# Kernel tuning notes

Measured on AMD Instinct MI355X. Metric: run time of the kernel, lower is better.

Reference implementation:

```python
import jax, jax.numpy as jnp
import numpy as np

N_NODES = 100000
N_EDGES = 1600000
IN_C, HID_C, OUT_C = 128, 128, 64


def gcn_conv(x, src, dst, n_nodes, W, b):
    # PyG GCNConv (normalize=True, add_self_loops=True):
    # out = D^{-1/2} (A+I) D^{-1/2} (x @ W^T) + b
    h = x @ W.T                                   # [N, out]
    deg = jax.ops.segment_sum(jnp.ones(src.shape, x.dtype), dst,
                              num_segments=n_nodes)  # includes self-loops
    dinv = jnp.where(deg > 0, jax.lax.rsqrt(deg), 0.0)
    norm = dinv[src] * dinv[dst]                  # [E+N]
    msg = h[src] * norm[:, None]                  # gather + scale
    out = jax.ops.segment_sum(msg, dst, num_segments=n_nodes)
    return out + b


def setup_inputs() -> dict:
    key = jax.random.key(0)
    ks = jax.random.split(key, 8)
    x = jax.random.normal(ks[0], (N_NODES, IN_C), dtype=jnp.float32)
    edge_index = jax.random.randint(ks[1], (2, N_EDGES), 0, N_NODES, dtype=jnp.int64)

    def lin(k, fan_out, fan_in):
        s = 1.0 / np.sqrt(fan_in)
        kw, kb = jax.random.split(k)
        W = jax.random.uniform(kw, (fan_out, fan_in), jnp.float32, -s, s)
        b = jax.random.uniform(kb, (fan_out,), jnp.float32, -s, s)
        return W, b

    W1, b1 = lin(ks[2], HID_C, IN_C)
    W2, b2 = lin(ks[3], HID_C, HID_C)
    W3, b3 = lin(ks[4], OUT_C, HID_C)
    return {"x": x, "edge_index": edge_index,
            "W1": W1, "b1": b1, "W2": W2, "b2": b2, "W3": W3, "b3": b3}


def reference(x, edge_index, W1, b1, W2, b2, W3, b3):
    n = x.shape[0]
    loop = jnp.arange(n, dtype=edge_index.dtype)
    src = jnp.concatenate([edge_index[0], loop])  # add self-loops once; identical per layer
    dst = jnp.concatenate([edge_index[1], loop])
    h = gcn_conv(x, src, dst, n, W1, b1)
    h = jax.nn.relu(h)
    h = gcn_conv(h, src, dst, n, W2, b2)
    h = jax.nn.relu(h)
    h = gcn_conv(h, src, dst, n, W3, b3)
    return h
```

## Files before the change

kernel.cpp:

```cpp
#include <hip/hip_runtime.h>


#define NPB 256
#define CAP 4672
#define BIN_WGS 512

typedef short bfrag __attribute__((ext_vector_type(8)));
typedef float f32x4 __attribute__((ext_vector_type(4)));
typedef unsigned short u16x8 __attribute__((ext_vector_type(8)));

__global__ __launch_bounds__(256) void init_cur(int* __restrict__ cur, int B) {
  int i = blockIdx.x * 256 + threadIdx.x;
  if (i < B) cur[i] = i * CAP;
}

__global__ __launch_bounds__(256) void bin_edges(const int* __restrict__ src,
                                                 const int* __restrict__ dst,
                                                 int* __restrict__ cur,
                                                 int* __restrict__ binned,
                                                 int E, int B) {
  __shared__ int lc[512];
  __shared__ int lbase[512];
  const int t = threadIdx.x;
  const int chunk = (E + BIN_WGS - 1) / BIN_WGS;
  const int e0 = blockIdx.x * chunk;
  const int e1 = min(E, e0 + chunk);

  for (int i = t; i < B; i += 256) lc[i] = 0;
  __syncthreads();
  for (int e = e0 + t; e < e1; e += 256) {
    int d = dst[e];
    atomicAdd(&lc[d >> 8], 1);
  }
  __syncthreads();
  for (int i = t; i < B; i += 256) {
    int c = lc[i];
    lbase[i] = c ? atomicAdd(&cur[i], c) : 0;
    lc[i] = 0;
  }
  __syncthreads();
  for (int e = e0 + t; e < e1; e += 256) {
    int d = dst[e];
    int s = __builtin_nontemporal_load(&src[e]);
    int bk = d >> 8;
    int p = lbase[bk] + atomicAdd(&lc[bk], 1);
    if (p < (bk + 1) * CAP)
      binned[p] = ((d & 255) << 24) | s;
  }
}

__global__ __launch_bounds__(256) void build_buckets(const int* __restrict__ binned,
                                                     const int* __restrict__ cur,
                                                     int* __restrict__ cols,
                                                     int2* __restrict__ off2,
                                                     float* __restrict__ dinv,
                                                     int N) {
  __shared__ int eb[CAP];
  __shared__ int ob[CAP];
  __shared__ int lc[256];
  __shared__ int sc[256];
  const int b = blockIdx.x;
  const int t = threadIdx.x;
  const int base = b * CAP;
  const int cntb = min(cur[b] - base, CAP);

  for (int i = t; i < cntb; i += 256) eb[i] = binned[base + i];
  lc[t] = 0;
  __syncthreads();
  for (int i = t; i < cntb; i += 256)
    atomicAdd(&lc[(unsigned)eb[i] >> 24], 1);
  __syncthreads();
  int myc = lc[t];
  sc[t] = myc;
  __syncthreads();
  for (int d = 1; d < 256; d <<= 1) {
    int a = (t >= d) ? sc[t - d] : 0;
    __syncthreads();
    sc[t] += a;
    __syncthreads();
  }
  int excl = sc[t] - myc;
  int node = b * NPB + t;
  if (node < N) {
    off2[node] = make_int2(base + excl, base + excl + myc);
    dinv[node] = rsqrtf((float)(myc + 1));
  }
  lc[t] = excl;
  __syncthreads();
  for (int i = t; i < cntb; i += 256) {
    int e = eb[i];
    int p = atomicAdd(&lc[(unsigned)e >> 24], 1);
    ob[p] = e & 0xFFFFFF;
  }
  __syncthreads();
  for (int i = t; i < cntb; i += 256) cols[base + i] = ob[i];
}

__device__ inline unsigned short bf16rne(float x) {
  unsigned u = __float_as_uint(x);
  return (unsigned short)((u + 0x7FFFu + ((u >> 16) & 1u)) >> 16);
}
__device__ inline float bf16lo(unsigned q) { return __uint_as_float(q << 16); }
__device__ inline float bf16hi(unsigned q) { return __uint_as_float(q & 0xFFFF0000u); }

__global__ __launch_bounds__(256) void split_w3(const float* __restrict__ W1,
                                                const float* __restrict__ W2,
                                                const float* __restrict__ W3,
                                                unsigned short* __restrict__ w1h,
                                                unsigned short* __restrict__ w1l,
                                                unsigned short* __restrict__ w2h,
                                                unsigned short* __restrict__ w2l,
                                                unsigned short* __restrict__ w3h,
                                                unsigned short* __restrict__ w3l) {
  int i = blockIdx.x * 256 + threadIdx.x;
  const float* W;
  unsigned short *hi, *lo;
  int j;
  if (i < 16384) {
    W = W1; hi = w1h; lo = w1l; j = i;
  } else if (i < 32768) {
    W = W2; hi = w2h; lo = w2l; j = i - 16384;
  } else if (i < 40960) {
    W = W3; hi = w3h; lo = w3l; j = i - 32768;
  } else {
    return;
  }
  float v = W[j];
  unsigned short h = bf16rne(v);
  hi[j] = h;
  lo[j] = bf16rne(v - __uint_as_float((unsigned)h << 16));
}

__global__ __launch_bounds__(256) void split_x(const float* __restrict__ X,
                                               unsigned short* __restrict__ xh,
                                               unsigned short* __restrict__ xl,
                                               int total8) {
  int i = blockIdx.x * 256 + threadIdx.x;
  if (i >= total8) return;
  const float4* px = (const float4*)(X + (size_t)i * 8);
  float4 v0 = px[0], v1 = px[1];
  float vv[8] = {v0.x, v0.y, v0.z, v0.w, v1.x, v1.y, v1.z, v1.w};
  u16x8 hv, lv;
#pragma unroll
  for (int j = 0; j < 8; ++j) {
    unsigned short h = bf16rne(vv[j]);
    hv[j] = h;
    lv[j] = bf16rne(vv[j] - __uint_as_float((unsigned)h << 16));
  }
  __builtin_nontemporal_store(hv, (u16x8*)(xh + (size_t)i * 8));
  __builtin_nontemporal_store(lv, (u16x8*)(xl + (size_t)i * 8));
}

#define LDP 136
template <int OUTC>
__global__ __launch_bounds__(256) void gemm_planes(const unsigned short* __restrict__ Xh,
                                                   const unsigned short* __restrict__ Xl,
                                                   const unsigned short* __restrict__ Whg,
                                                   const unsigned short* __restrict__ Wlg,
                                                   const float* __restrict__ dinv,
                                                   unsigned short* __restrict__ Y,
                                                   int M) {
  constexpr int CHUNKS = OUTC / 64;
  __shared__ unsigned short Whi[64 * LDP], Wlo[64 * LDP];
  const int tid = threadIdx.x;
  const int bx = blockIdx.x;
  const int m_base = (bx / CHUNKS) * 64;
  const int cc = (bx % CHUNKS) * 64;

  for (int idx = tid; idx < 64 * 16; idx += 256) {
    int r = idx >> 4, g = idx & 15;
    *(u16x8*)(Whi + r * LDP + g * 8) =
        *(const u16x8*)(Whg + (size_t)(cc + r) * 128 + g * 8);
    *(u16x8*)(Wlo + r * LDP + g * 8) =
        *(const u16x8*)(Wlg + (size_t)(cc + r) * 128 + g * 8);
  }
  __syncthreads();

  const int lane = tid & 63;
  const int wv = tid >> 6;
  const int col_l = lane & 15;
  const int quad = lane >> 4;
  const size_t arow = (size_t)min(m_base + wv * 16 + col_l, M - 1) * 128;
  const int bBase = col_l * LDP + quad * 8;

  bfrag aH[4], aL[4];
#pragma unroll
  for (int ks = 0; ks < 4; ++ks) {
    aH[ks] = *(const bfrag*)(Xh + arow + ks * 32 + quad * 8);
    aL[ks] = *(const bfrag*)(Xl + arow + ks * 32 + quad * 8);
  }

  f32x4 acc[4] = {{0.f, 0.f, 0.f, 0.f},
                  {0.f, 0.f, 0.f, 0.f},
                  {0.f, 0.f, 0.f, 0.f},
                  {0.f, 0.f, 0.f, 0.f}};
#pragma unroll
  for (int ks = 0; ks < 4; ++ks) {
#pragma unroll
    for (int t = 0; t < 4; ++t) {
      int bo = bBase + t * 16 * LDP + ks * 32;
      bfrag bHi = *(const bfrag*)(Whi + bo);
      bfrag bLo = *(const bfrag*)(Wlo + bo);
      acc[t] = __builtin_amdgcn_mfma_f32_16x16x32_bf16(aH[ks], bHi, acc[t], 0, 0, 0);
      acc[t] = __builtin_amdgcn_mfma_f32_16x16x32_bf16(aL[ks], bHi, acc[t], 0, 0, 0);
      acc[t] = __builtin_amdgcn_mfma_f32_16x16x32_bf16(aH[ks], bLo, acc[t], 0, 0, 0);
    }
  }

#pragma unroll
  for (int r = 0; r < 4; ++r) {
    int row = m_base + wv * 16 + quad * 4 + r;
    if (row < M) {
      float s = dinv[row];
#pragma unroll
      for (int t = 0; t < 4; ++t) {
        unsigned short h = bf16rne(acc[t][r] * s);
        Y[(size_t)row * OUTC + cc + t * 16 + col_l] = h;
      }
    }
  }
}

template <int C, bool RELU, bool SPLIT>
__global__ __launch_bounds__(256) void aggregate3(const unsigned short* __restrict__ xs,
                                                  const int2* __restrict__ off2,
                                                  const int* __restrict__ cols,
                                                  const float* __restrict__ dinv,
                                                  const float* __restrict__ bias,
                                                  float* __restrict__ outf,
                                                  unsigned short* __restrict__ oh,
                                                  unsigned short* __restrict__ ol,
                                                  int N) {
  constexpr int CG = C / 8;
  constexpr int EG = 64 / CG;
  int wid = (int)((blockIdx.x * blockDim.x + threadIdx.x) >> 6);
  int lane = threadIdx.x & 63;
  if (wid >= N) return;
  const int eg = lane / CG;
  const int cg = lane % CG;

  float acc[8] = {0.f, 0.f, 0.f, 0.f, 0.f, 0.f, 0.f, 0.f};
  if (eg == 0) {
    uint4 d = *(const uint4*)(xs + (size_t)wid * C + cg * 8);
    acc[0] = bf16lo(d.x); acc[1] = bf16hi(d.x);
    acc[2] = bf16lo(d.y); acc[3] = bf16hi(d.y);
    acc[4] = bf16lo(d.z); acc[5] = bf16hi(d.z);
    acc[6] = bf16lo(d.w); acc[7] = bf16hi(d.w);
  }

  int2 oo = off2[wid];
  int ebase = oo.x;
  const int eend = oo.y;
  while (ebase < eend) {
    int cnt = eend - ebase;
    if (cnt > 64) cnt = 64;
    int col = (lane < cnt) ? __builtin_nontemporal_load(&cols[ebase + lane]) : 0;
    const int c1 = cnt - 1;
    for (int j = 0; j < cnt; j += 4 * EG) {
      int i0 = j + eg, i1 = i0 + EG, i2 = i1 + EG, i3 = i2 + EG;
      int s0 = __shfl(col, min(i0, c1));
      int s1 = __shfl(col, min(i1, c1));
      int s2 = __shfl(col, min(i2, c1));
      int s3 = __shfl(col, min(i3, c1));
      uint4 d0 = *(const uint4*)(xs + (size_t)s0 * C + cg * 8);
      uint4 d1 = *(const uint4*)(xs + (size_t)s1 * C + cg * 8);
      uint4 d2 = *(const uint4*)(xs + (size_t)s2 * C + cg * 8);
      uint4 d3 = *(const uint4*)(xs + (size_t)s3 * C + cg * 8);
      if (i0 < cnt) {
        acc[0] += bf16lo(d0.x); acc[1] += bf16hi(d0.x);
        acc[2] += bf16lo(d0.y); acc[3] += bf16hi(d0.y);
        acc[4] += bf16lo(d0.z); acc[5] += bf16hi(d0.z);
        acc[6] += bf16lo(d0.w); acc[7] += bf16hi(d0.w);
      }
      if (i1 < cnt) {
        acc[0] += bf16lo(d1.x); acc[1] += bf16hi(d1.x);
        acc[2] += bf16lo(d1.y); acc[3] += bf16hi(d1.y);
        acc[4] += bf16lo(d1.z); acc[5] += bf16hi(d1.z);
        acc[6] += bf16lo(d1.w); acc[7] += bf16hi(d1.w);
      }
      if (i2 < cnt) {
        acc[0] += bf16lo(d2.x); acc[1] += bf16hi(d2.x);
        acc[2] += bf16lo(d2.y); acc[3] += bf16hi(d2.y);
        acc[4] += bf16lo(d2.z); acc[5] += bf16hi(d2.z);
        acc[6] += bf16lo(d2.w); acc[7] += bf16hi(d2.w);
      }
      if (i3 < cnt) {
        acc[0] += bf16lo(d3.x); acc[1] += bf16hi(d3.x);
        acc[2] += bf16lo(d3.y); acc[3] += bf16hi(d3.y);
        acc[4] += bf16lo(d3.z); acc[5] += bf16hi(d3.z);
        acc[6] += bf16lo(d3.w); acc[7] += bf16hi(d3.w);
      }
    }
    ebase += cnt;
  }

#pragma unroll
  for (int m = CG; m < 64; m <<= 1) {
#pragma unroll
    for (int q = 0; q < 8; ++q) acc[q] += __shfl_xor(acc[q], m);
  }

  if (eg == 0) {
    float dd = dinv[wid];
    const float4 bA = *(const float4*)(bias + cg * 8);
    const float4 bB = *(const float4*)(bias + cg * 8 + 4);
    float h[8];
    h[0] = acc[0] * dd + bA.x; h[1] = acc[1] * dd + bA.y;
    h[2] = acc[2] * dd + bA.z; h[3] = acc[3] * dd + bA.w;
    h[4] = acc[4] * dd + bB.x; h[5] = acc[5] * dd + bB.y;
    h[6] = acc[6] * dd + bB.z; h[7] = acc[7] * dd + bB.w;
    if (RELU) {
#pragma unroll
      for (int q = 0; q < 8; ++q) h[q] = fmaxf(h[q], 0.f);
    }
    if (SPLIT) {
      u16x8 hv, lv;
#pragma unroll
      for (int q = 0; q < 8; ++q) {
        unsigned short hb = bf16rne(h[q]);
        hv[q] = hb;
        lv[q] = bf16rne(h[q] - __uint_as_float((unsigned)hb << 16));
      }
      __builtin_nontemporal_store(hv, (u16x8*)(oh + (size_t)wid * C + cg * 8));
      __builtin_nontemporal_store(lv, (u16x8*)(ol + (size_t)wid * C + cg * 8));
    } else {
      f32x4 oA = {h[0], h[1], h[2], h[3]};
      f32x4 oB = {h[4], h[5], h[6], h[7]};
      __builtin_nontemporal_store(oA, (f32x4*)(outf + (size_t)wid * C + cg * 8));
      __builtin_nontemporal_store(oB, (f32x4*)(outf + (size_t)wid * C + cg * 8 + 4));
    }
  }
}


extern "C" void kernel_launch(void* const* d_in, const int* in_sizes, int n_in,
                              void* d_out, int out_size, void* d_ws, size_t ws_size,
                              hipStream_t stream) {
  const float* x  = (const float*)d_in[0];
  const int*   ei = (const int*)d_in[1];
  const float* W1 = (const float*)d_in[2];
  const float* b1 = (const float*)d_in[3];
  const float* W2 = (const float*)d_in[4];
  const float* b2 = (const float*)d_in[5];
  const float* W3 = (const float*)d_in[6];
  const float* b3 = (const float*)d_in[7];

  const int N = in_sizes[0] / 128;
  const int E = in_sizes[1] / 2;
  const int* src = ei;
  const int* dst = ei + E;
  const int B = (N + NPB - 1) / NPB;

  char* w = (char*)d_ws;
  size_t p = 0;
  auto alloc = [&](size_t bytes) -> void* {
    void* r = w + p;
    p = (p + bytes + 255) & ~(size_t)255;
    return r;
  };
  float*    dinv   = (float*)alloc((size_t)N * 4);
  int2*     off2   = (int2*)alloc((size_t)N * 8);
  int*      cur    = (int*)alloc((size_t)B * 4);
  int*      binned = (int*)alloc((size_t)B * CAP * 4);
  int*      cols   = (int*)alloc((size_t)B * CAP * 4);
  unsigned short* xsb = (unsigned short*)alloc((size_t)N * 128 * 2);
  unsigned short* hh  = (unsigned short*)alloc((size_t)N * 128 * 2);
  unsigned short* hl  = (unsigned short*)alloc((size_t)N * 128 * 2);
  unsigned short* w1h = (unsigned short*)alloc(128 * 128 * 2);
  unsigned short* w1l = (unsigned short*)alloc(128 * 128 * 2);
  unsigned short* w2h = (unsigned short*)alloc(128 * 128 * 2);
  unsigned short* w2l = (unsigned short*)alloc(128 * 128 * 2);
  unsigned short* w3h = (unsigned short*)alloc(64 * 128 * 2);
  unsigned short* w3l = (unsigned short*)alloc(64 * 128 * 2);
  unsigned short* xh  = (unsigned short*)alloc((size_t)N * 128 * 2);
  unsigned short* xl  = (unsigned short*)alloc((size_t)N * 128 * 2);

  init_cur<<<(B + 255) / 256, 256, 0, stream>>>(cur, B);
  bin_edges<<<BIN_WGS, 256, 0, stream>>>(src, dst, cur, binned, E, B);
  split_w3<<<160, 256, 0, stream>>>(W1, W2, W3, w1h, w1l, w2h, w2l, w3h, w3l);
  split_x<<<(N * 16 + 255) / 256, 256, 0, stream>>>(x, xh, xl, N * 16);
  build_buckets<<<B, 256, 0, stream>>>(binned, cur, cols, off2, dinv, N);

  const int gb = (N + 63) / 64;
  const int ab = (N + 3) / 4;

  gemm_planes<128><<<gb * 2, 256, 0, stream>>>(xh, xl, w1h, w1l, dinv, xsb, N);
  aggregate3<128, true, true><<<ab, 256, 0, stream>>>(xsb, off2, cols, dinv, b1,
                                                      nullptr, hh, hl, N);
  gemm_planes<128><<<gb * 2, 256, 0, stream>>>(hh, hl, w2h, w2l, dinv, xsb, N);
  aggregate3<128, true, true><<<ab, 256, 0, stream>>>(xsb, off2, cols, dinv, b2,
                                                      nullptr, hh, hl, N);
  gemm_planes<64><<<gb, 256, 0, stream>>>(hh, hl, w3h, w3l, dinv, xsb, N);
  aggregate3<64, false, false><<<ab, 256, 0, stream>>>(xsb, off2, cols, dinv, b3,
                                                       (float*)d_out, nullptr,
                                                       nullptr, N);
}
```

Before: 420.3 us.

## Fuse x bf16 split into first GEMM and map aggregation to sub-wave groups per node

Drops the separate split_x kernel and its two bf16 plane buffers; the first GEMM now reads fp32 x directly and splits it into hi/lo bf16 fragments in registers. The aggregation kernel is restructured so each node is handled by a group of C/8 lanes instead of a full 64-lane wavefront, which removes the cross-lane reduction and puts several nodes in each wave. This avoids a full read/write pass over x and the wasted lanes when a node has few edges (average degree about 17). In exchange, lanes within a wave can diverge when neighbouring nodes have different degrees.

```diff
diff --git a/kernel.cpp b/kernel.cpp
--- a/kernel.cpp
+++ b/kernel.cpp
@@ -131,27 +131,8 @@
   lo[j] = bf16rne(v - __uint_as_float((unsigned)h << 16));
 }
 
-__global__ __launch_bounds__(256) void split_x(const float* __restrict__ X,
-                                               unsigned short* __restrict__ xh,
-                                               unsigned short* __restrict__ xl,
-                                               int total8) {
-  int i = blockIdx.x * 256 + threadIdx.x;
-  if (i >= total8) return;
-  const float4* px = (const float4*)(X + (size_t)i * 8);
-  float4 v0 = px[0], v1 = px[1];
-  float vv[8] = {v0.x, v0.y, v0.z, v0.w, v1.x, v1.y, v1.z, v1.w};
-  u16x8 hv, lv;
-#pragma unroll
-  for (int j = 0; j < 8; ++j) {
-    unsigned short h = bf16rne(vv[j]);
-    hv[j] = h;
-    lv[j] = bf16rne(vv[j] - __uint_as_float((unsigned)h << 16));
-  }
-  __builtin_nontemporal_store(hv, (u16x8*)(xh + (size_t)i * 8));
-  __builtin_nontemporal_store(lv, (u16x8*)(xl + (size_t)i * 8));
-}
-
 #define LDP 136
+
 template <int OUTC>
 __global__ __launch_bounds__(256) void gemm_planes(const unsigned short* __restrict__ Xh,
                                                    const unsigned short* __restrict__ Xl,
@@ -221,8 +202,90 @@
   }
 }
 
+template <int OUTC>
+__global__ __launch_bounds__(256) void gemm_xsplit(const float* __restrict__ X,
+                                                   const unsigned short* __restrict__ Whg,
+                                                   const unsigned short* __restrict__ Wlg,
+                                                   const float* __restrict__ dinv,
+                                                   unsigned short* __restrict__ Y,
+                                                   int M) {
+  constexpr int CHUNKS = OUTC / 64;
+  __shared__ unsigned short Whi[64 * LDP], Wlo[64 * LDP];
+  const int tid = threadIdx.x;
+  const int bx = blockIdx.x;
+  const int m_base = (bx / CHUNKS) * 64;
+  const int cc = (bx % CHUNKS) * 64;
+
+  for (int idx = tid; idx < 64 * 16; idx += 256) {
+    int r = idx >> 4, g = idx & 15;
+    *(u16x8*)(Whi + r * LDP + g * 8) =
+        *(const u16x8*)(Whg + (size_t)(cc + r) * 128 + g * 8);
+    *(u16x8*)(Wlo + r * LDP + g * 8) =
+        *(const u16x8*)(Wlg + (size_t)(cc + r) * 128 + g * 8);
+  }
+  __syncthreads();
+
+  const int lane = tid & 63;
+  const int wv = tid >> 6;
+  const int col_l = lane & 15;
+  const int quad = lane >> 4;
+  const size_t arow = (size_t)min(m_base + wv * 16 + col_l, M - 1) * 128;
+  const int bBase = col_l * LDP + quad * 8;
+
+  bfrag aH[4], aL[4];
+#pragma unroll
+  for (int ks = 0; ks < 4; ++ks) {
+    float4 v0 = *(const float4*)(X + arow + ks * 32 + quad * 8);
+    float4 v1 = *(const float4*)(X + arow + ks * 32 + quad * 8 + 4);
+    float vv[8] = {v0.x, v0.y, v0.z, v0.w, v1.x, v1.y, v1.z, v1.w};
+#pragma unroll
+    for (int j = 0; j < 8; ++j) {
+      unsigned short h = bf16rne(vv[j]);
+      aH[ks][j] = (short)h;
+      aL[ks][j] = (short)bf16rne(vv[j] - __uint_as_float((unsigned)h << 16));
+    }
+  }
+
+  f32x4 acc[4] = {{0.f, 0.f, 0.f, 0.f},
+                  {0.f, 0.f, 0.f, 0.f},
+                  {0.f, 0.f, 0.f, 0.f},
+                  {0.f, 0.f, 0.f, 0.f}};
+#pragma unroll
+  for (int ks = 0; ks < 4; ++ks) {
+#pragma unroll
+    for (int t = 0; t < 4; ++t) {
+      int bo = bBase + t * 16 * LDP + ks * 32;
+      bfrag bHi = *(const bfrag*)(Whi + bo);
+      bfrag bLo = *(const bfrag*)(Wlo + bo);
+      acc[t] = __builtin_amdgcn_mfma_f32_16x16x32_bf16(aH[ks], bHi, acc[t], 0, 0, 0);
+      acc[t] = __builtin_amdgcn_mfma_f32_16x16x32_bf16(aL[ks], bHi, acc[t], 0, 0, 0);
+      acc[t] = __builtin_amdgcn_mfma_f32_16x16x32_bf16(aH[ks], bLo, acc[t], 0, 0, 0);
+    }
+  }
+
+#pragma unroll
+  for (int r = 0; r < 4; ++r) {
+    int row = m_base + wv * 16 + quad * 4 + r;
+    if (row < M) {
+      float s = dinv[row];
+#pragma unroll
+      for (int t = 0; t < 4; ++t) {
+        unsigned short h = bf16rne(acc[t][r] * s);
+        Y[(size_t)row * OUTC + cc + t * 16 + col_l] = h;
+      }
+    }
+  }
+}
+
+__device__ inline void acc_add(float* a, uint4 d) {
+  a[0] += bf16lo(d.x); a[1] += bf16hi(d.x);
+  a[2] += bf16lo(d.y); a[3] += bf16hi(d.y);
+  a[4] += bf16lo(d.z); a[5] += bf16hi(d.z);
+  a[6] += bf16lo(d.w); a[7] += bf16hi(d.w);
+}
+
 template <int C, bool RELU, bool SPLIT>
-__global__ __launch_bounds__(256) void aggregate3(const unsigned short* __restrict__ xs,
+__global__ __launch_bounds__(256) void aggregate4(const unsigned short* __restrict__ xs,
                                                   const int2* __restrict__ off2,
                                                   const int* __restrict__ cols,
                                                   const float* __restrict__ dinv,
@@ -231,104 +294,75 @@
                                                   unsigned short* __restrict__ oh,
                                                   unsigned short* __restrict__ ol,
                                                   int N) {
-  constexpr int CG = C / 8;
-  constexpr int EG = 64 / CG;
-  int wid = (int)((blockIdx.x * blockDim.x + threadIdx.x) >> 6);
-  int lane = threadIdx.x & 63;
-  if (wid >= N) return;
-  const int eg = lane / CG;
-  const int cg = lane % CG;
-
-  float acc[8] = {0.f, 0.f, 0.f, 0.f, 0.f, 0.f, 0.f, 0.f};
-  if (eg == 0) {
-    uint4 d = *(const uint4*)(xs + (size_t)wid * C + cg * 8);
+  constexpr int GL = C / 8;
+  constexpr int LSH = (GL == 16) ? 4 : 3;
+  constexpr int NPBk = 256 / GL;
+  const int t = threadIdx.x;
+  const int gl = t & (GL - 1);
+  const int node = blockIdx.x * NPBk + (t >> LSH);
+  if (node >= N) return;
+
+  const unsigned co = (unsigned)gl * 16;
+
+  float acc[8];
+  {
+    uint4 d = *(const uint4*)((const char*)xs + (size_t)node * (C * 2) + co);
     acc[0] = bf16lo(d.x); acc[1] = bf16hi(d.x);
     acc[2] = bf16lo(d.y); acc[3] = bf16hi(d.y);
     acc[4] = bf16lo(d.z); acc[5] = bf16hi(d.z);
     acc[6] = bf16lo(d.w); acc[7] = bf16hi(d.w);
   }
 
-  int2 oo = off2[wid];
-  int ebase = oo.x;
-  const int eend = oo.y;
-  while (ebase < eend) {
-    int cnt = eend - ebase;
-    if (cnt > 64) cnt = 64;
-    int col = (lane < cnt) ? __builtin_nontemporal_load(&cols[ebase + lane]) : 0;
-    const int c1 = cnt - 1;
-    for (int j = 0; j < cnt; j += 4 * EG) {
-      int i0 = j + eg, i1 = i0 + EG, i2 = i1 + EG, i3 = i2 + EG;
-      int s0 = __shfl(col, min(i0, c1));
-      int s1 = __shfl(col, min(i1, c1));
-      int s2 = __shfl(col, min(i2, c1));
-      int s3 = __shfl(col, min(i3, c1));
-      uint4 d0 = *(const uint4*)(xs + (size_t)s0 * C + cg * 8);
-      uint4 d1 = *(const uint4*)(xs + (size_t)s1 * C + cg * 8);
-      uint4 d2 = *(const uint4*)(xs + (size_t)s2 * C + cg * 8);
-      uint4 d3 = *(const uint4*)(xs + (size_t)s3 * C + cg * 8);
-      if (i0 < cnt) {
-        acc[0] += bf16lo(d0.x); acc[1] += bf16hi(d0.x);
-        acc[2] += bf16lo(d0.y); acc[3] += bf16hi(d0.y);
-        acc[4] += bf16lo(d0.z); acc[5] += bf16hi(d0.z);
-        acc[6] += bf16lo(d0.w); acc[7] += bf16hi(d0.w);
-      }
-      if (i1 < cnt) {
-        acc[0] += bf16lo(d1.x); acc[1] += bf16hi(d1.x);
-        acc[2] += bf16lo(d1.y); acc[3] += bf16hi(d1.y);
-        acc[4] += bf16lo(d1.z); acc[5] += bf16hi(d1.z);
-        acc[6] += bf16lo(d1.w); acc[7] += bf16hi(d1.w);
-      }
-      if (i2 < cnt) {
-        acc[0] += bf16lo(d2.x); acc[1] += bf16hi(d2.x);
-        acc[2] += bf16lo(d2.y); acc[3] += bf16hi(d2.y);
-        acc[4] += bf16lo(d2.z); acc[5] += bf16hi(d2.z);
-        acc[6] += bf16lo(d2.w); acc[7] += bf16hi(d2.w);
-      }
-      if (i3 < cnt) {
-        acc[0] += bf16lo(d3.x); acc[1] += bf16hi(d3.x);
-        acc[2] += bf16lo(d3.y); acc[3] += bf16hi(d3.y);
-        acc[4] += bf16lo(d3.z); acc[5] += bf16hi(d3.z);
-        acc[6] += bf16lo(d3.w); acc[7] += bf16hi(d3.w);
-      }
-    }
-    ebase += cnt;
-  }
-
-#pragma unroll
-  for (int m = CG; m < 64; m <<= 1) {
-#pragma unroll
-    for (int q = 0; q < 8; ++q) acc[q] += __shfl_xor(acc[q], m);
-  }
-
-  if (eg == 0) {
-    float dd = dinv[wid];
-    const float4 bA = *(const float4*)(bias + cg * 8);
-    const float4 bB = *(const float4*)(bias + cg * 8 + 4);
-    float h[8];
-    h[0] = acc[0] * dd + bA.x; h[1] = acc[1] * dd + bA.y;
-    h[2] = acc[2] * dd + bA.z; h[3] = acc[3] * dd + bA.w;
-    h[4] = acc[4] * dd + bB.x; h[5] = acc[5] * dd + bB.y;
-    h[6] = acc[6] * dd + bB.z; h[7] = acc[7] * dd + bB.w;
-    if (RELU) {
-#pragma unroll
-      for (int q = 0; q < 8; ++q) h[q] = fmaxf(h[q], 0.f);
-    }
-    if (SPLIT) {
-      u16x8 hv, lv;
-#pragma unroll
-      for (int q = 0; q < 8; ++q) {
-        unsigned short hb = bf16rne(h[q]);
-        hv[q] = hb;
-        lv[q] = bf16rne(h[q] - __uint_as_float((unsigned)hb << 16));
-      }
-      __builtin_nontemporal_store(hv, (u16x8*)(oh + (size_t)wid * C + cg * 8));
-      __builtin_nontemporal_store(lv, (u16x8*)(ol + (size_t)wid * C + cg * 8));
-    } else {
-      f32x4 oA = {h[0], h[1], h[2], h[3]};
-      f32x4 oB = {h[4], h[5], h[6], h[7]};
-      __builtin_nontemporal_store(oA, (f32x4*)(outf + (size_t)wid * C + cg * 8));
-      __builtin_nontemporal_store(oB, (f32x4*)(outf + (size_t)wid * C + cg * 8 + 4));
-    }
+  const int2 oo = off2[node];
+  const int en = oo.y;
+  for (int e0 = oo.x; e0 < en; e0 += GL) {
+    int col = __builtin_nontemporal_load(&cols[min(e0 + gl, en - 1)]);
+    int m = en - e0;
+    if (m > GL) m = GL;
+    const int c1 = m - 1;
+    for (int j = 0; j < m; j += 4) {
+      int s0 = __shfl(col, min(j,     c1), GL);
+      int s1 = __shfl(col, min(j + 1, c1), GL);
+      int s2 = __shfl(col, min(j + 2, c1), GL);
+      int s3 = __shfl(col, min(j + 3, c1), GL);
+      uint4 d0 = *(const uint4*)((const char*)xs + (size_t)s0 * (C * 2) + co);
+      uint4 d1 = *(const uint4*)((const char*)xs + (size_t)s1 * (C * 2) + co);
+      uint4 d2 = *(const uint4*)((const char*)xs + (size_t)s2 * (C * 2) + co);
+      uint4 d3 = *(const uint4*)((const char*)xs + (size_t)s3 * (C * 2) + co);
+      acc_add(acc, d0);
+      if (j + 1 < m) acc_add(acc, d1);
+      if (j + 2 < m) acc_add(acc, d2);
+      if (j + 3 < m) acc_add(acc, d3);
+    }
+  }
+
+  const float dd = dinv[node];
+  const float4 bA = *(const float4*)(bias + gl * 8);
+  const float4 bB = *(const float4*)(bias + gl * 8 + 4);
+  float h[8];
+  h[0] = acc[0] * dd + bA.x; h[1] = acc[1] * dd + bA.y;
+  h[2] = acc[2] * dd + bA.z; h[3] = acc[3] * dd + bA.w;
+  h[4] = acc[4] * dd + bB.x; h[5] = acc[5] * dd + bB.y;
+  h[6] = acc[6] * dd + bB.z; h[7] = acc[7] * dd + bB.w;
+  if (RELU) {
+#pragma unroll
+    for (int q = 0; q < 8; ++q) h[q] = fmaxf(h[q], 0.f);
+  }
+  if (SPLIT) {
+    u16x8 hv, lv;
+#pragma unroll
+    for (int q = 0; q < 8; ++q) {
+      unsigned short hb = bf16rne(h[q]);
+      hv[q] = hb;
+      lv[q] = bf16rne(h[q] - __uint_as_float((unsigned)hb << 16));
+    }
+    __builtin_nontemporal_store(hv, (u16x8*)(oh + (size_t)node * C + gl * 8));
+    __builtin_nontemporal_store(lv, (u16x8*)(ol + (size_t)node * C + gl * 8));
+  } else {
+    f32x4 oA = {h[0], h[1], h[2], h[3]};
+    f32x4 oB = {h[4], h[5], h[6], h[7]};
+    __builtin_nontemporal_store(oA, (f32x4*)(outf + (size_t)node * C + gl * 8));
+    __builtin_nontemporal_store(oB, (f32x4*)(outf + (size_t)node * C + gl * 8 + 4));
   }
 }
 
@@ -372,26 +406,24 @@
   unsigned short* w2l = (unsigned short*)alloc(128 * 128 * 2);
   unsigned short* w3h = (unsigned short*)alloc(64 * 128 * 2);
   unsigned short* w3l = (unsigned short*)alloc(64 * 128 * 2);
-  unsigned short* xh  = (unsigned short*)alloc((size_t)N * 128 * 2);
-  unsigned short* xl  = (unsigned short*)alloc((size_t)N * 128 * 2);
 
   init_cur<<<(B + 255) / 256, 256, 0, stream>>>(cur, B);
   bin_edges<<<BIN_WGS, 256, 0, stream>>>(src, dst, cur, binned, E, B);
   split_w3<<<160, 256, 0, stream>>>(W1, W2, W3, w1h, w1l, w2h, w2l, w3h, w3l);
-  split_x<<<(N * 16 + 255) / 256, 256, 0, stream>>>(x, xh, xl, N * 16);
   build_buckets<<<B, 256, 0, stream>>>(binned, cur, cols, off2, dinv, N);
 
   const int gb = (N + 63) / 64;
-  const int ab = (N + 3) / 4;
-
-  gemm_planes<128><<<gb * 2, 256, 0, stream>>>(xh, xl, w1h, w1l, dinv, xsb, N);
-  aggregate3<128, true, true><<<ab, 256, 0, stream>>>(xsb, off2, cols, dinv, b1,
-                                                      nullptr, hh, hl, N);
+  const int ab128 = (N + 15) / 16;
+  const int ab64  = (N + 31) / 32;
+
+  gemm_xsplit<128><<<gb * 2, 256, 0, stream>>>(x, w1h, w1l, dinv, xsb, N);
+  aggregate4<128, true, true><<<ab128, 256, 0, stream>>>(xsb, off2, cols, dinv, b1,
+                                                         nullptr, hh, hl, N);
   gemm_planes<128><<<gb * 2, 256, 0, stream>>>(hh, hl, w2h, w2l, dinv, xsb, N);
-  aggregate3<128, true, true><<<ab, 256, 0, stream>>>(xsb, off2, cols, dinv, b2,
-                                                      nullptr, hh, hl, N);
+  aggregate4<128, true, true><<<ab128, 256, 0, stream>>>(xsb, off2, cols, dinv, b2,
+                                                         nullptr, hh, hl, N);
   gemm_planes<64><<<gb, 256, 0, stream>>>(hh, hl, w3h, w3l, dinv, xsb, N);
-  aggregate3<64, false, false><<<ab, 256, 0, stream>>>(xsb, off2, cols, dinv, b3,
-                                                       (float*)d_out, nullptr,
-                                                       nullptr, N);
-}
+  aggregate4<64, false, false><<<ab64, 256, 0, stream>>>(xsb, off2, cols, dinv, b3,
+                                                         (float*)d_out, nullptr,
+                                                         nullptr, N);
+}
```

New measurement: 386.0 us. 1.09x faster.
